# Optimization experiments

Measured on AMD Instinct MI355X. Metric: run time of the kernel, lower is better.

Reference implementation:

```python
import jax, jax.numpy as jnp
import numpy as np

N_NODES = 100000
N_EDGES = 1600000
HID = 128
N_GRAPHS = 512
MAX_Z = 1000
NODE_VOCAB = 200000
OUT = 2
BN_EPS = 1e-5


def setup_inputs() -> dict:
    key = jax.random.key(0)
    ks = jax.random.split(key, 20)

    def w(k, shape, fan_in):
        return jax.random.normal(k, shape, dtype=jnp.float32) / np.sqrt(fan_in)

    inp = {
        "num_nodes": N_NODES,
        "z": jax.random.randint(ks[0], (N_NODES,), 0, MAX_Z),
        "edge_index": jax.random.randint(ks[1], (2, N_EDGES), 0, N_NODES),
        "batch": jnp.sort(jax.random.randint(ks[2], (N_NODES,), 0, N_GRAPHS)),
        "node_id": jax.random.randint(ks[3], (N_NODES,), 0, NODE_VOCAB),
        # parameters
        "z_emb": jax.random.normal(ks[4], (MAX_Z, HID), dtype=jnp.float32) * 0.02,
        "node_emb": jax.random.normal(ks[5], (NODE_VOCAB, HID), dtype=jnp.float32) * 0.02,
        "W0": w(ks[6], (2 * HID, HID), 2 * HID), "b0": jnp.zeros((HID,), jnp.float32),
        "W1": w(ks[7], (HID, HID), HID), "b1": jnp.zeros((HID,), jnp.float32),
        "W2": w(ks[8], (HID, HID), HID), "b2": jnp.zeros((HID,), jnp.float32),
        "mlp_W1": w(ks[9], (HID, HID), HID), "mlp_b1": jnp.zeros((HID,), jnp.float32),
        "bn_gamma": jnp.ones((HID,), jnp.float32), "bn_beta": jnp.zeros((HID,), jnp.float32),
        "mlp_W2": w(ks[10], (HID, OUT), HID), "mlp_b2": jnp.zeros((OUT,), jnp.float32),
    }
    return inp


def _gin_conv(x, src, dst, W, b, num_nodes):
    # GINConv(eps=0): out_i = Linear(x_i + sum_{j->i} x_j)
    agg = jax.ops.segment_sum(x[src], dst, num_segments=num_nodes)
    return (x + agg) @ W + b


def reference(num_nodes, z, edge_index, batch, node_id,
              z_emb, node_emb, W0, b0, W1, b1, W2, b2,
              mlp_W1, mlp_b1, bn_gamma, bn_beta, mlp_W2, mlp_b2):
    src, dst = edge_index[0], edge_index[1]
    # node features: concat(z_embedding(z), node_embedding(node_id)) -> [N, 2H]
    x = jnp.concatenate([z_emb[z], node_emb[node_id]], axis=1)

    x = jax.nn.relu(_gin_conv(x, src, dst, W0, b0, num_nodes))  # [N, H]
    x = jax.nn.relu(_gin_conv(x, src, dst, W1, b1, num_nodes))
    x = _gin_conv(x, src, dst, W2, b2, num_nodes)  # last conv: no relu

    # global mean pool over graphs
    sums = jax.ops.segment_sum(x, batch, num_segments=N_GRAPHS)  # [G, H]
    counts = jax.ops.segment_sum(jnp.ones((num_nodes,), x.dtype), batch,
                                 num_segments=N_GRAPHS)
    pooled = sums / jnp.maximum(counts, 1.0)[:, None]

    # MLP([H, H, OUT]): Linear -> BatchNorm(eval, identity stats) -> ReLU -> Linear
    h = pooled @ mlp_W1 + mlp_b1
    h = h * (bn_gamma / np.sqrt(1.0 + BN_EPS)) + bn_beta
    h = jax.nn.relu(h)
    return h @ mlp_W2 + mlp_b2  # [G, OUT]
```

## Files before the change

### kernel.cpp

```cpp
#include <hip/hip_runtime.h>

#define NN 100000
#define NE 1600000
#define HID 128
#define NG 512
#define MAXZ 1000
#define NBK 256
#define BK_S 391
#define TILE_E 2048
#define PSL 8

typedef unsigned short u16;
typedef unsigned int u32;
typedef __attribute__((ext_vector_type(8))) short bf16x8;
typedef __attribute__((ext_vector_type(4))) float f32x4;

__device__ __forceinline__ u16 bf16r(float x) {
    u32 u = __float_as_uint(x);
    u32 r = (u + 0x7fffu + ((u >> 16) & 1u)) >> 16;
    return (u16)r;
}
__device__ __forceinline__ float bflo(u32 u) { return __uint_as_float(u << 16); }
__device__ __forceinline__ float bfhi(u32 u) { return __uint_as_float(u & 0xffff0000u); }

#define ACC8(v) { \
    acc[0] += bflo((v).x); acc[1] += bfhi((v).x); \
    acc[2] += bflo((v).y); acc[3] += bfhi((v).y); \
    acc[4] += bflo((v).z); acc[5] += bfhi((v).z); \
    acc[6] += bflo((v).w); acc[7] += bfhi((v).w); }

__global__ __launch_bounds__(256) void bucket_count_kernel(const int* __restrict__ dst,
                                                           int* __restrict__ bcount) {
    __shared__ int lh[NBK];
    int t = threadIdx.x;
    lh[t] = 0;
    __syncthreads();
    int stride = gridDim.x * 256;
    for (int i = blockIdx.x * 256 + t; i < NE; i += stride)
        atomicAdd(&lh[dst[i] / BK_S], 1);
    __syncthreads();
    int v = lh[t];
    if (v) atomicAdd(&bcount[t], v);
}

__global__ __launch_bounds__(NBK) void scan_nbk_kernel(const int* __restrict__ bcount,
                                                       int* __restrict__ boff,
                                                       int* __restrict__ gcursor) {
    __shared__ int buf[NBK];
    int t = threadIdx.x;
    int v = bcount[t];
    buf[t] = v;
    __syncthreads();
    for (int d = 1; d < NBK; d <<= 1) {
        int add = (t >= d) ? buf[t - d] : 0;
        __syncthreads();
        buf[t] += add;
        __syncthreads();
    }
    int excl = buf[t] - v;
    boff[t] = excl;
    gcursor[t] = excl;
    if (t == NBK - 1) boff[NBK] = buf[NBK - 1];
}

__global__ __launch_bounds__(256) void pair_scatter_kernel(const int* __restrict__ src,
                                                           const int* __restrict__ dst,
                                                           int* __restrict__ gcursor,
                                                           u32* __restrict__ pairs) {
    __shared__ int cnt[NBK];
    __shared__ int base[NBK];
    int t = threadIdx.x;
    long tile0 = (long)blockIdx.x * TILE_E;
    cnt[t] = 0;
    __syncthreads();
    u32 val[8], br[8];
#pragma unroll
    for (int i = 0; i < 8; ++i) {
        long idx = tile0 + i * 256 + t;
        val[i] = 0xFFFFFFFFu;
        if (idx < NE) {
            int d = dst[idx];
            int b = d / BK_S;
            int r = atomicAdd(&cnt[b], 1);
            val[i] = ((u32)(d - b * BK_S) << 17) | (u32)src[idx];
            br[i] = ((u32)b << 12) | (u32)r;
        }
    }
    __syncthreads();
    int c = cnt[t];
    if (c) base[t] = atomicAdd(&gcursor[t], c);
    __syncthreads();
#pragma unroll
    for (int i = 0; i < 8; ++i) {
        if (val[i] != 0xFFFFFFFFu) {
            u32 b = br[i] >> 12, r = br[i] & 0xFFFu;
            pairs[base[b] + r] = val[i];
        }
    }
}

__global__ __launch_bounds__(256) void bucket_build_kernel(const u32* __restrict__ pairs,
                                                           const int* __restrict__ boff,
                                                           int* __restrict__ off,
                                                           int* __restrict__ csr) {
    __shared__ int lh[BK_S];
    __shared__ int ts[256];
    int b = blockIdx.x, t = threadIdx.x;
    int base = boff[b], end = boff[b + 1];
    int node0 = b * BK_S;
    for (int i = t; i < BK_S; i += 256) lh[i] = 0;
    __syncthreads();
    for (int j = base + t; j < end; j += 256)
        atomicAdd(&lh[pairs[j] >> 17], 1);
    __syncthreads();
    int i0 = t * 2, i1 = t * 2 + 1;
    int c0 = (i0 < BK_S) ? lh[i0] : 0;
    int c1 = (i1 < BK_S) ? lh[i1] : 0;
    int s = c0 + c1;
    ts[t] = s;
    __syncthreads();
    for (int d = 1; d < 256; d <<= 1) {
        int add = (t >= d) ? ts[t - d] : 0;
        __syncthreads();
        ts[t] += add;
        __syncthreads();
    }
    int e0 = base + ts[t] - s;
    int e1 = e0 + c0;
    if (i0 < BK_S) { lh[i0] = e0; int n = node0 + i0; if (n < NN) off[n] = e0; }
    if (i1 < BK_S) { lh[i1] = e1; int n = node0 + i1; if (n < NN) off[n] = e1; }
    if (b == 0 && t == 0) off[NN] = NE;
    __syncthreads();
    for (int j = base + t; j < end; j += 256) {
        u32 p = pairs[j];
        int pos = atomicAdd(&lh[p >> 17], 1);
        csr[pos] = (int)(p & 0x1FFFFu);
    }
}

__global__ __launch_bounds__(128) void wt2_kernel(const float* __restrict__ W0b, const float* __restrict__ W1,
                                                  u16* __restrict__ W0bt, u16* __restrict__ W1t) {
    int k = blockIdx.x & 127;
    int which = blockIdx.x >> 7;
    int n = threadIdx.x;
    const float* W = which ? W1 : W0b;
    u16* o = which ? W1t : W0bt;
    o[n * HID + k] = bf16r(W[k * HID + n]);
}

#define FMA4(acc, s, w) { acc.x += (s)*(w).x; acc.y += (s)*(w).y; acc.z += (s)*(w).z; acc.w += (s)*(w).w; }
__global__ __launch_bounds__(256) void gemm128_kernel(
    const float* __restrict__ X, const float* __restrict__ W,
    float* __restrict__ Y, int nrows)
{
    __shared__ float xs[32][132];
    int t = threadIdx.x;
    int row0 = blockIdx.x * 32;
    int sr = t >> 5;
    int sk = (t & 31) * 4;
#pragma unroll
    for (int p = 0; p < 4; ++p) {
        int r = p * 8 + sr;
        int grow = row0 + r;
        float4 v = make_float4(0.f, 0.f, 0.f, 0.f);
        if (grow < nrows) v = *(const float4*)(X + (long)grow * HID + sk);
        *(float4*)(&xs[r][sk]) = v;
    }
    __syncthreads();
    int cg = t & 31, rg = t >> 5;
    int c = cg * 4, r = rg * 4;
    float4 a0 = make_float4(0,0,0,0), a1 = a0, a2 = a0, a3 = a0;
    for (int k = 0; k < 128; k += 4) {
        float x0[4], x1[4], x2[4], x3[4];
        *(float4*)x0 = *(const float4*)&xs[r + 0][k];
        *(float4*)x1 = *(const float4*)&xs[r + 1][k];
        *(float4*)x2 = *(const float4*)&xs[r + 2][k];
        *(float4*)x3 = *(const float4*)&xs[r + 3][k];
#pragma unroll
        for (int j = 0; j < 4; ++j) {
            float4 w = *(const float4*)(W + (k + j) * HID + c);
            FMA4(a0, x0[j], w); FMA4(a1, x1[j], w); FMA4(a2, x2[j], w); FMA4(a3, x3[j], w);
        }
    }
    float4 accs[4] = {a0, a1, a2, a3};
#pragma unroll
    for (int i = 0; i < 4; ++i) {
        int grow = row0 + r + i;
        if (grow < nrows) *(float4*)(Y + (long)grow * HID + c) = accs[i];
    }
}

template<int SRC_BF16>
__global__ __launch_bounds__(256) void mfma_gemm_kernel(
    const void* __restrict__ Xsrc,
    const int* __restrict__ gatherIdx,
    const u16* __restrict__ Wt,
    const float* __restrict__ addTab, const int* __restrict__ addIdx,
    u16* __restrict__ Y, int nrows)
{
    __shared__ u16 Als[64][136];
    __shared__ u16 Wls[128][136];
    int t = threadIdx.x;
    int row0 = blockIdx.x * 64;

#pragma unroll
    for (int p = 0; p < 2; ++p) {
        int n = p * 64 + (t >> 2);
        int k0 = (t & 3) * 32;
        const u16* src = Wt + n * HID + k0;
        uint4 v0 = *(const uint4*)(src);
        uint4 v1 = *(const uint4*)(src + 8);
        uint4 v2 = *(const uint4*)(src + 16);
        uint4 v3 = *(const uint4*)(src + 24);
        *(uint4*)&Wls[n][k0]      = v0;
        *(uint4*)&Wls[n][k0 + 8]  = v1;
        *(uint4*)&Wls[n][k0 + 16] = v2;
        *(uint4*)&Wls[n][k0 + 24] = v3;
    }

    if (SRC_BF16) {
        const u16* X = (const u16*)Xsrc;
#pragma unroll
        for (int p = 0; p < 4; ++p) {
            int r = p * 16 + (t >> 4);
            int k0 = (t & 15) * 8;
            int grow = row0 + r;
            uint4 v = make_uint4(0, 0, 0, 0);
            if (grow < nrows) {
                long srow = gatherIdx ? (long)gatherIdx[grow] : (long)grow;
                v = *(const uint4*)(X + srow * HID + k0);
            }
            *(uint4*)&Als[r][k0] = v;
        }
    } else {
        const float* X = (const float*)Xsrc;
#pragma unroll
        for (int p = 0; p < 8; ++p) {
            int r = p * 8 + (t >> 5);
            int k0 = (t & 31) * 4;
            int grow = row0 + r;
            float4 v = make_float4(0.f, 0.f, 0.f, 0.f);
            if (grow < nrows) {
                long srow = gatherIdx ? (long)gatherIdx[grow] : (long)grow;
                v = *(const float4*)(X + srow * HID + k0);
            }
            ushort4 b;
            b.x = bf16r(v.x); b.y = bf16r(v.y); b.z = bf16r(v.z); b.w = bf16r(v.w);
            *(ushort4*)&Als[r][k0] = b;
        }
    }
    __syncthreads();

    int w = t >> 6, l = t & 63;
    int lr = l & 15, lq = l >> 4;
    f32x4 acc[8];
#pragma unroll
    for (int i = 0; i < 8; ++i) acc[i] = (f32x4){0.f, 0.f, 0.f, 0.f};

#pragma unroll
    for (int kk = 0; kk < 4; ++kk) {
        bf16x8 af = *(const bf16x8*)&Als[w * 16 + lr][kk * 32 + lq * 8];
#pragma unroll
        for (int nt = 0; nt < 8; ++nt) {
            bf16x8 bf = *(const bf16x8*)&Wls[nt * 16 + lr][kk * 32 + lq * 8];
            acc[nt] = __builtin_amdgcn_mfma_f32_16x16x32_bf16(af, bf, acc[nt], 0, 0, 0);
        }
    }

    int orow = row0 + w * 16 + lq * 4;
#pragma unroll
    for (int r = 0; r < 4; ++r) {
        int grow = orow + r;
        if (grow < nrows) {
            const float* ap = addTab ? (addTab + (long)addIdx[grow] * HID) : nullptr;
#pragma unroll
            for (int nt = 0; nt < 8; ++nt) {
                int col = nt * 16 + lr;
                float v = acc[nt][r];
                if (ap) v += ap[col];
                Y[(long)grow * HID + col] = bf16r(v);
            }
        }
    }
}

__global__ __launch_bounds__(256) void aggregate_kernel(
    const u16* __restrict__ H, u16* __restrict__ Xo,
    const int* __restrict__ off, const int* __restrict__ csr,
    const float* __restrict__ bias, int n, int doRelu)
{
    int node = blockIdx.x * 4 + (threadIdx.x >> 6);
    if (node >= n) return;
    int lane = threadIdx.x & 63;
    int g = lane >> 4, fl = lane & 15;
    int s = off[node], e = off[node + 1];

    float acc[8] = {0.f, 0.f, 0.f, 0.f, 0.f, 0.f, 0.f, 0.f};
    int j = s + g;

    for (; j + 12 < e; j += 16) {
        int i0 = csr[j];
        int i1 = csr[j + 4];
        int i2 = csr[j + 8];
        int i3 = csr[j + 12];
        uint4 v0 = *(const uint4*)(H + (long)i0 * HID + fl * 8);
        uint4 v1 = *(const uint4*)(H + (long)i1 * HID + fl * 8);
        uint4 v2 = *(const uint4*)(H + (long)i2 * HID + fl * 8);
        uint4 v3 = *(const uint4*)(H + (long)i3 * HID + fl * 8);
        ACC8(v0); ACC8(v1); ACC8(v2); ACC8(v3);
    }
    for (; j + 4 < e; j += 8) {
        int i0 = csr[j];
        int i1 = csr[j + 4];
        uint4 v0 = *(const uint4*)(H + (long)i0 * HID + fl * 8);
        uint4 v1 = *(const uint4*)(H + (long)i1 * HID + fl * 8);
        ACC8(v0); ACC8(v1);
    }
    if (j < e) {
        int i0 = csr[j];
        uint4 v0 = *(const uint4*)(H + (long)i0 * HID + fl * 8);
        ACC8(v0);
    }

#pragma unroll
    for (int i = 0; i < 8; ++i) {
        acc[i] += __shfl_xor(acc[i], 16);
        acc[i] += __shfl_xor(acc[i], 32);
    }

    if (g == 0) {
        uint4 sv = *(const uint4*)(H + (long)node * HID + fl * 8);
        float4 ba = *(const float4*)(bias + fl * 8);
        float4 bb = *(const float4*)(bias + fl * 8 + 4);
        float r[8];
        r[0] = acc[0] + bflo(sv.x) + ba.x;
        r[1] = acc[1] + bfhi(sv.x) + ba.y;
        r[2] = acc[2] + bflo(sv.y) + ba.z;
        r[3] = acc[3] + bfhi(sv.y) + ba.w;
        r[4] = acc[4] + bflo(sv.z) + bb.x;
        r[5] = acc[5] + bfhi(sv.z) + bb.y;
        r[6] = acc[6] + bflo(sv.w) + bb.z;
        r[7] = acc[7] + bfhi(sv.w) + bb.w;
        if (doRelu) {
#pragma unroll
            for (int i = 0; i < 8; ++i) r[i] = fmaxf(r[i], 0.f);
        }
        uint4 ov;
        ov.x = (u32)bf16r(r[0]) | ((u32)bf16r(r[1]) << 16);
        ov.y = (u32)bf16r(r[2]) | ((u32)bf16r(r[3]) << 16);
        ov.z = (u32)bf16r(r[4]) | ((u32)bf16r(r[5]) << 16);
        ov.w = (u32)bf16r(r[6]) | ((u32)bf16r(r[7]) << 16);
        *(uint4*)(Xo + (long)node * HID + fl * 8) = ov;
    }
}

__global__ __launch_bounds__(256) void edgepool_kernel(
    const u16* __restrict__ X, const int* __restrict__ batch,
    const int* __restrict__ off, const int* __restrict__ csr,
    float* __restrict__ poolPart)
{
    __shared__ float red[4][HID];
    int g = blockIdx.x >> 3;
    int sl = blockIdx.x & (PSL - 1);
    int t = threadIdx.x;
    int grp = t >> 4, fl = t & 15;
    int lo = 0, hi = NN;
    while (lo < hi) { int m = (lo + hi) >> 1; if (batch[m] < g) lo = m + 1; else hi = m; }
    int ns = lo;
    lo = 0; hi = NN;
    while (lo < hi) { int m = (lo + hi) >> 1; if (batch[m] < g + 1) lo = m + 1; else hi = m; }
    int ne = lo;
    int es = off[ns], ee = off[ne];

    int nn = ne - ns, en = ee - es;
    int ns0 = ns + (int)((long)nn * sl / PSL);
    int ne0 = ns + (int)((long)nn * (sl + 1) / PSL);
    int es0 = es + (int)((long)en * sl / PSL);
    int ee0 = es + (int)((long)en * (sl + 1) / PSL);

    float acc[8] = {0.f, 0.f, 0.f, 0.f, 0.f, 0.f, 0.f, 0.f};
    for (int i = ns0 + grp; i < ne0; i += 16) {
        uint4 v = *(const uint4*)(X + (long)i * HID + fl * 8);
        ACC8(v);
    }
    int j = es0 + grp;
    for (; j + 48 < ee0; j += 64) {
        int i0 = csr[j];
        int i1 = csr[j + 16];
        int i2 = csr[j + 32];
        int i3 = csr[j + 48];
        uint4 v0 = *(const uint4*)(X + (long)i0 * HID + fl * 8);
        uint4 v1 = *(const uint4*)(X + (long)i1 * HID + fl * 8);
        uint4 v2 = *(const uint4*)(X + (long)i2 * HID + fl * 8);
        uint4 v3 = *(const uint4*)(X + (long)i3 * HID + fl * 8);
        ACC8(v0); ACC8(v1); ACC8(v2); ACC8(v3);
    }
    for (; j < ee0; j += 16) {
        int i0 = csr[j];
        uint4 v0 = *(const uint4*)(X + (long)i0 * HID + fl * 8);
        ACC8(v0);
    }

#pragma unroll
    for (int i = 0; i < 8; ++i) {
        acc[i] += __shfl_xor(acc[i], 16);
        acc[i] += __shfl_xor(acc[i], 32);
    }
    int w = t >> 6, lane = t & 63;
    if (lane < 16) {
#pragma unroll
        for (int i = 0; i < 8; ++i) red[w][lane * 8 + i] = acc[i];
    }
    __syncthreads();
    if (t < HID) {
        float v = red[0][t] + red[1][t] + red[2][t] + red[3][t];
        poolPart[((long)g * PSL + sl) * HID + t] = v;
    }
}

__global__ __launch_bounds__(128) void mlp_kernel(
    const float* __restrict__ poolPart, const int* __restrict__ batch,
    const float* __restrict__ W2f, const float* __restrict__ b2,
    const float* __restrict__ W1, const float* __restrict__ b1,
    const float* __restrict__ gamma, const float* __restrict__ beta,
    const float* __restrict__ mW2, const float* __restrict__ mb2, float* __restrict__ out)
{
    int g = blockIdx.x, t = threadIdx.x;
    __shared__ float pt[HID];
    __shared__ float p[HID];
    __shared__ float red[4];
    int lo = 0, hi = NN;
    while (lo < hi) { int m = (lo + hi) >> 1; if (batch[m] < g) lo = m + 1; else hi = m; }
    int ns = lo;
    lo = 0; hi = NN;
    while (lo < hi) { int m = (lo + hi) >> 1; if (batch[m] < g + 1) lo = m + 1; else hi = m; }
    float cnt = fmaxf((float)(lo - ns), 1.f);

    float v = 0.f;
#pragma unroll
    for (int s = 0; s < PSL; ++s) v += poolPart[((long)g * PSL + s) * HID + t];
    pt[t] = v / cnt;
    __syncthreads();
    float pv = b2[t];
    for (int k = 0; k < HID; ++k) pv += pt[k] * W2f[k * HID + t];
    p[t] = pv;
    __syncthreads();
    float acc = b1[t];
    for (int k = 0; k < HID; ++k) acc += p[k] * W1[k * HID + t];
    const float inv = 1.0f / sqrtf(1.0f + 1e-5f);
    acc = acc * (gamma[t] * inv) + beta[t];
    acc = fmaxf(acc, 0.f);
    float v0 = acc * mW2[t * 2 + 0];
    float v1 = acc * mW2[t * 2 + 1];
    for (int d = 32; d > 0; d >>= 1) { v0 += __shfl_down(v0, d); v1 += __shfl_down(v1, d); }
    int w = t >> 6, lane = t & 63;
    if (lane == 0) { red[w * 2] = v0; red[w * 2 + 1] = v1; }
    __syncthreads();
    if (t == 0) {
        out[g * 2 + 0] = red[0] + red[2] + mb2[0];
        out[g * 2 + 1] = red[1] + red[3] + mb2[1];
    }
}

extern "C" void kernel_launch(void* const* d_in, const int* in_sizes, int n_in,
                              void* d_out, int out_size, void* d_ws, size_t ws_size,
                              hipStream_t stream) {
    const int*   z        = (const int*)d_in[1];
    const int*   ei       = (const int*)d_in[2];
    const int*   batch    = (const int*)d_in[3];
    const int*   node_id  = (const int*)d_in[4];
    const float* z_emb    = (const float*)d_in[5];
    const float* node_emb = (const float*)d_in[6];
    const float* W0  = (const float*)d_in[7];
    const float* b0  = (const float*)d_in[8];
    const float* W1  = (const float*)d_in[9];
    const float* b1  = (const float*)d_in[10];
    const float* W2  = (const float*)d_in[11];
    const float* b2  = (const float*)d_in[12];
    const float* mW1 = (const float*)d_in[13];
    const float* mb1 = (const float*)d_in[14];
    const float* gam = (const float*)d_in[15];
    const float* bet = (const float*)d_in[16];
    const float* mW2 = (const float*)d_in[17];
    const float* mb2 = (const float*)d_in[18];
    float* out = (float*)d_out;

    const int* srcArr = ei;
    const int* dstArr = ei + NE;

    char* ws = (char*)d_ws;
    size_t o = 0;
    auto alloc = [&](size_t bytes) { char* p = ws + o; o += (bytes + 255) & ~(size_t)255; return p; };
    u16*   A      = (u16*)alloc((size_t)NN * HID * 2);
    u16*   B      = (u16*)alloc((size_t)NN * HID * 2);
    float* zW     = (float*)alloc((size_t)MAXZ * HID * 4);
    u16*   W0bt   = (u16*)alloc((size_t)HID * HID * 2);
    u16*   W1t    = (u16*)alloc((size_t)HID * HID * 2);
    int*   bcount = (int*)alloc((size_t)NBK * 4);
    int*   boff   = (int*)alloc((size_t)(NBK + 1) * 4);
    int*   gcur   = (int*)alloc((size_t)NBK * 4);
    u32*   pairs  = (u32*)alloc((size_t)NE * 4);
    int*   off    = (int*)alloc((size_t)(NN + 1) * 4);
    int*   csr    = (int*)alloc((size_t)NE * 4);
    float* poolP  = (float*)alloc((size_t)NG * PSL * HID * 4);
    (void)ws_size;

    hipMemsetAsync(bcount, 0, (size_t)NBK * 4, stream);
    bucket_count_kernel<<<1024, 256, 0, stream>>>(dstArr, bcount);
    scan_nbk_kernel<<<1, NBK, 0, stream>>>(bcount, boff, gcur);
    pair_scatter_kernel<<<(NE + TILE_E - 1) / TILE_E, 256, 0, stream>>>(srcArr, dstArr, gcur, pairs);
    bucket_build_kernel<<<NBK, 256, 0, stream>>>(pairs, boff, off, csr);

    wt2_kernel<<<2 * HID, HID, 0, stream>>>(W0 + HID * HID, W1, W0bt, W1t);

    gemm128_kernel<<<(MAXZ + 31) / 32, 256, 0, stream>>>(z_emb, W0, zW, MAXZ);

    const int GB = (NN + 63) / 64;
    mfma_gemm_kernel<0><<<GB, 256, 0, stream>>>(node_emb, node_id, W0bt, zW, z, B, NN);
    aggregate_kernel<<<NN / 4, 256, 0, stream>>>(B, A, off, csr, b0, NN, 1);
    mfma_gemm_kernel<1><<<GB, 256, 0, stream>>>(A, nullptr, W1t, nullptr, nullptr, B, NN);
    aggregate_kernel<<<NN / 4, 256, 0, stream>>>(B, A, off, csr, b1, NN, 1);
    edgepool_kernel<<<NG * PSL, 256, 0, stream>>>(A, batch, off, csr, poolP);
    mlp_kernel<<<NG, 128, 0, stream>>>(poolP, batch, W2, b2, mW1, mb1, gam, bet, mW2, mb2, out);
}
```

Before: 352.6 us.

## Replace bucket count/scan with fixed-capacity bucket slots and per-node end array

Removes the bucket histogram and scan kernels by giving each destination bucket a fixed-capacity slot (CAP entries) in the pairs and CSR arrays, so scatter only needs an atomic per-bucket cursor. Because buckets are no longer contiguous, each node now stores an explicit end offset, and the aggregate and pool kernels read start/end per node. The pool kernel changes from a flat edge-range split to a per-node loop over neighbors, which may lower load balance and memory-level parallelism there. It also assumes no bucket exceeds 8192 edges; the average is about 6250, so a skewed destination distribution would overflow.

```diff
diff --git a/kernel.cpp b/kernel.cpp
--- a/kernel.cpp
+++ b/kernel.cpp
@@ -8,6 +8,7 @@
 #define NBK 256
 #define BK_S 391
 #define TILE_E 2048
+#define CAP 8192
 #define PSL 8
 
 typedef unsigned short u16;
@@ -29,43 +30,9 @@
     acc[4] += bflo((v).z); acc[5] += bfhi((v).z); \
     acc[6] += bflo((v).w); acc[7] += bfhi((v).w); }
 
-__global__ __launch_bounds__(256) void bucket_count_kernel(const int* __restrict__ dst,
-                                                           int* __restrict__ bcount) {
-    __shared__ int lh[NBK];
-    int t = threadIdx.x;
-    lh[t] = 0;
-    __syncthreads();
-    int stride = gridDim.x * 256;
-    for (int i = blockIdx.x * 256 + t; i < NE; i += stride)
-        atomicAdd(&lh[dst[i] / BK_S], 1);
-    __syncthreads();
-    int v = lh[t];
-    if (v) atomicAdd(&bcount[t], v);
-}
-
-__global__ __launch_bounds__(NBK) void scan_nbk_kernel(const int* __restrict__ bcount,
-                                                       int* __restrict__ boff,
-                                                       int* __restrict__ gcursor) {
-    __shared__ int buf[NBK];
-    int t = threadIdx.x;
-    int v = bcount[t];
-    buf[t] = v;
-    __syncthreads();
-    for (int d = 1; d < NBK; d <<= 1) {
-        int add = (t >= d) ? buf[t - d] : 0;
-        __syncthreads();
-        buf[t] += add;
-        __syncthreads();
-    }
-    int excl = buf[t] - v;
-    boff[t] = excl;
-    gcursor[t] = excl;
-    if (t == NBK - 1) boff[NBK] = buf[NBK - 1];
-}
-
 __global__ __launch_bounds__(256) void pair_scatter_kernel(const int* __restrict__ src,
                                                            const int* __restrict__ dst,
-                                                           int* __restrict__ gcursor,
+                                                           int* __restrict__ gcount,
                                                            u32* __restrict__ pairs) {
     __shared__ int cnt[NBK];
     __shared__ int base[NBK];
@@ -88,30 +55,32 @@
     }
     __syncthreads();
     int c = cnt[t];
-    if (c) base[t] = atomicAdd(&gcursor[t], c);
+    if (c) base[t] = atomicAdd(&gcount[t], c);
     __syncthreads();
 #pragma unroll
     for (int i = 0; i < 8; ++i) {
         if (val[i] != 0xFFFFFFFFu) {
             u32 b = br[i] >> 12, r = br[i] & 0xFFFu;
-            pairs[base[b] + r] = val[i];
+            pairs[(long)b * CAP + base[b] + r] = val[i];
         }
     }
 }
 
 __global__ __launch_bounds__(256) void bucket_build_kernel(const u32* __restrict__ pairs,
-                                                           const int* __restrict__ boff,
+                                                           const int* __restrict__ gcount,
                                                            int* __restrict__ off,
+                                                           int* __restrict__ endA,
                                                            int* __restrict__ csr) {
     __shared__ int lh[BK_S];
     __shared__ int ts[256];
     int b = blockIdx.x, t = threadIdx.x;
-    int base = boff[b], end = boff[b + 1];
+    int base = b * CAP;
+    int cnt = gcount[b];
     int node0 = b * BK_S;
     for (int i = t; i < BK_S; i += 256) lh[i] = 0;
     __syncthreads();
-    for (int j = base + t; j < end; j += 256)
-        atomicAdd(&lh[pairs[j] >> 17], 1);
+    for (int j = t; j < cnt; j += 256)
+        atomicAdd(&lh[pairs[base + j] >> 17], 1);
     __syncthreads();
     int i0 = t * 2, i1 = t * 2 + 1;
     int c0 = (i0 < BK_S) ? lh[i0] : 0;
@@ -127,12 +96,11 @@
     }
     int e0 = base + ts[t] - s;
     int e1 = e0 + c0;
-    if (i0 < BK_S) { lh[i0] = e0; int n = node0 + i0; if (n < NN) off[n] = e0; }
-    if (i1 < BK_S) { lh[i1] = e1; int n = node0 + i1; if (n < NN) off[n] = e1; }
-    if (b == 0 && t == 0) off[NN] = NE;
-    __syncthreads();
-    for (int j = base + t; j < end; j += 256) {
-        u32 p = pairs[j];
+    if (i0 < BK_S) { lh[i0] = e0; int n = node0 + i0; if (n < NN) { off[n] = e0; endA[n] = e0 + c0; } }
+    if (i1 < BK_S) { lh[i1] = e1; int n = node0 + i1; if (n < NN) { off[n] = e1; endA[n] = e1 + c1; } }
+    __syncthreads();
+    for (int j = t; j < cnt; j += 256) {
+        u32 p = pairs[base + j];
         int pos = atomicAdd(&lh[p >> 17], 1);
         csr[pos] = (int)(p & 0x1FFFFu);
     }
@@ -286,14 +254,14 @@
 
 __global__ __launch_bounds__(256) void aggregate_kernel(
     const u16* __restrict__ H, u16* __restrict__ Xo,
-    const int* __restrict__ off, const int* __restrict__ csr,
+    const int* __restrict__ off, const int* __restrict__ endA, const int* __restrict__ csr,
     const float* __restrict__ bias, int n, int doRelu)
 {
     int node = blockIdx.x * 4 + (threadIdx.x >> 6);
     if (node >= n) return;
     int lane = threadIdx.x & 63;
     int g = lane >> 4, fl = lane & 15;
-    int s = off[node], e = off[node + 1];
+    int s = off[node], e = endA[node];
 
     float acc[8] = {0.f, 0.f, 0.f, 0.f, 0.f, 0.f, 0.f, 0.f};
     int j = s + g;
@@ -356,7 +324,7 @@
 
 __global__ __launch_bounds__(256) void edgepool_kernel(
     const u16* __restrict__ X, const int* __restrict__ batch,
-    const int* __restrict__ off, const int* __restrict__ csr,
+    const int* __restrict__ off, const int* __restrict__ endA, const int* __restrict__ csr,
     float* __restrict__ poolPart)
 {
     __shared__ float red[4][HID];
@@ -370,35 +338,32 @@
     lo = 0; hi = NN;
     while (lo < hi) { int m = (lo + hi) >> 1; if (batch[m] < g + 1) lo = m + 1; else hi = m; }
     int ne = lo;
-    int es = off[ns], ee = off[ne];
-
-    int nn = ne - ns, en = ee - es;
+    int nn = ne - ns;
     int ns0 = ns + (int)((long)nn * sl / PSL);
     int ne0 = ns + (int)((long)nn * (sl + 1) / PSL);
-    int es0 = es + (int)((long)en * sl / PSL);
-    int ee0 = es + (int)((long)en * (sl + 1) / PSL);
 
     float acc[8] = {0.f, 0.f, 0.f, 0.f, 0.f, 0.f, 0.f, 0.f};
     for (int i = ns0 + grp; i < ne0; i += 16) {
         uint4 v = *(const uint4*)(X + (long)i * HID + fl * 8);
         ACC8(v);
-    }
-    int j = es0 + grp;
-    for (; j + 48 < ee0; j += 64) {
-        int i0 = csr[j];
-        int i1 = csr[j + 16];
-        int i2 = csr[j + 32];
-        int i3 = csr[j + 48];
-        uint4 v0 = *(const uint4*)(X + (long)i0 * HID + fl * 8);
-        uint4 v1 = *(const uint4*)(X + (long)i1 * HID + fl * 8);
-        uint4 v2 = *(const uint4*)(X + (long)i2 * HID + fl * 8);
-        uint4 v3 = *(const uint4*)(X + (long)i3 * HID + fl * 8);
-        ACC8(v0); ACC8(v1); ACC8(v2); ACC8(v3);
-    }
-    for (; j < ee0; j += 16) {
-        int i0 = csr[j];
-        uint4 v0 = *(const uint4*)(X + (long)i0 * HID + fl * 8);
-        ACC8(v0);
+        int s = off[i], e = endA[i];
+        int j = s;
+        for (; j + 3 < e; j += 4) {
+            int i0 = csr[j];
+            int i1 = csr[j + 1];
+            int i2 = csr[j + 2];
+            int i3 = csr[j + 3];
+            uint4 v0 = *(const uint4*)(X + (long)i0 * HID + fl * 8);
+            uint4 v1 = *(const uint4*)(X + (long)i1 * HID + fl * 8);
+            uint4 v2 = *(const uint4*)(X + (long)i2 * HID + fl * 8);
+            uint4 v3 = *(const uint4*)(X + (long)i3 * HID + fl * 8);
+            ACC8(v0); ACC8(v1); ACC8(v2); ACC8(v3);
+        }
+        for (; j < e; ++j) {
+            int i0 = csr[j];
+            uint4 v0 = *(const uint4*)(X + (long)i0 * HID + fl * 8);
+            ACC8(v0);
+        }
     }
 
 #pragma unroll
@@ -496,20 +461,17 @@
     float* zW     = (float*)alloc((size_t)MAXZ * HID * 4);
     u16*   W0bt   = (u16*)alloc((size_t)HID * HID * 2);
     u16*   W1t    = (u16*)alloc((size_t)HID * HID * 2);
-    int*   bcount = (int*)alloc((size_t)NBK * 4);
-    int*   boff   = (int*)alloc((size_t)(NBK + 1) * 4);
-    int*   gcur   = (int*)alloc((size_t)NBK * 4);
-    u32*   pairs  = (u32*)alloc((size_t)NE * 4);
-    int*   off    = (int*)alloc((size_t)(NN + 1) * 4);
-    int*   csr    = (int*)alloc((size_t)NE * 4);
+    int*   gcount = (int*)alloc((size_t)NBK * 4);
+    u32*   pairs  = (u32*)alloc((size_t)NBK * CAP * 4);
+    int*   off    = (int*)alloc((size_t)NN * 4);
+    int*   endA   = (int*)alloc((size_t)NN * 4);
+    int*   csr    = (int*)alloc((size_t)NBK * CAP * 4);
     float* poolP  = (float*)alloc((size_t)NG * PSL * HID * 4);
     (void)ws_size;
 
-    hipMemsetAsync(bcount, 0, (size_t)NBK * 4, stream);
-    bucket_count_kernel<<<1024, 256, 0, stream>>>(dstArr, bcount);
-    scan_nbk_kernel<<<1, NBK, 0, stream>>>(bcount, boff, gcur);
-    pair_scatter_kernel<<<(NE + TILE_E - 1) / TILE_E, 256, 0, stream>>>(srcArr, dstArr, gcur, pairs);
-    bucket_build_kernel<<<NBK, 256, 0, stream>>>(pairs, boff, off, csr);
+    hipMemsetAsync(gcount, 0, (size_t)NBK * 4, stream);
+    pair_scatter_kernel<<<(NE + TILE_E - 1) / TILE_E, 256, 0, stream>>>(srcArr, dstArr, gcount, pairs);
+    bucket_build_kernel<<<NBK, 256, 0, stream>>>(pairs, gcount, off, endA, csr);
 
     wt2_kernel<<<2 * HID, HID, 0, stream>>>(W0 + HID * HID, W1, W0bt, W1t);
 
@@ -517,9 +479,9 @@
 
     const int GB = (NN + 63) / 64;
     mfma_gemm_kernel<0><<<GB, 256, 0, stream>>>(node_emb, node_id, W0bt, zW, z, B, NN);
-    aggregate_kernel<<<NN / 4, 256, 0, stream>>>(B, A, off, csr, b0, NN, 1);
+    aggregate_kernel<<<NN / 4, 256, 0, stream>>>(B, A, off, endA, csr, b0, NN, 1);
     mfma_gemm_kernel<1><<<GB, 256, 0, stream>>>(A, nullptr, W1t, nullptr, nullptr, B, NN);
-    aggregate_kernel<<<NN / 4, 256, 0, stream>>>(B, A, off, csr, b1, NN, 1);
-    edgepool_kernel<<<NG * PSL, 256, 0, stream>>>(A, batch, off, csr, poolP);
+    aggregate_kernel<<<NN / 4, 256, 0, stream>>>(B, A, off, endA, csr, b1, NN, 1);
+    edgepool_kernel<<<NG * PSL, 256, 0, stream>>>(A, batch, off, endA, csr, poolP);
     mlp_kernel<<<NG, 128, 0, stream>>>(poolP, batch, W2, b2, mW1, mb1, gam, bet, mW2, mb2, out);
 }
```

After: 335.3 us. -4.9%, faster.
